# Kernel optimization log

Measured on AMD Instinct MI355X. Metric: run time of the kernel, lower is better.

## Reference

```python
import jax, jax.numpy as jnp
import numpy as np

B, S, K, H = 8192, 512, 8, 512  # batch, size_half, n_segments, hidden
EPS = 1e-6


def setup_inputs() -> dict:
    key = jax.random.key(0)
    k0, k1, k2, k3 = jax.random.split(key, 4)
    x_input = jax.random.uniform(k0, (B, 2 * S), dtype=jnp.float32)  # in [0,1)
    log_density = jax.random.normal(k1, (B, 1), dtype=jnp.float32)
    W1 = jax.random.normal(k2, (S, H), dtype=jnp.float32) / np.sqrt(S).astype(np.float32)
    b1 = jnp.zeros((H,), jnp.float32)
    W2 = jax.random.normal(k3, (H, S * (2 * K + 1)), dtype=jnp.float32) / np.sqrt(H).astype(np.float32)
    b2 = jnp.zeros((S * (2 * K + 1),), jnp.float32)
    return {"x_input": x_input, "log_density": log_density,
            "W1": W1, "b1": b1, "W2": W2, "b2": b2}


def reference(x_input, log_density, W1, b1, W2, b2):
    # even_sites=True: passive half a = first S cols, transformed half b = last S
    x_a = x_input[:, :S]
    x_b = x_input[:, S:]

    # NeuralNetwork: Linear -> tanh -> Linear -> tanh (final_activation == activation)
    hid = jnp.tanh((x_a - 0.5) @ W1 + b1)
    net = jnp.tanh(hid @ W2 + b2).reshape(-1, S, 2 * K + 1)  # [B,S,2K+1]
    h_raw, w_raw = net[..., :K + 1], net[..., K + 1:]

    w_norm = jax.nn.softmax(w_raw, axis=2)                       # [B,S,K]
    eh = jnp.exp(h_raw)                                          # [B,S,K+1]
    h_norm = eh / jnp.sum(0.5 * w_norm * (eh[..., :-1] + eh[..., 1:]),
                          axis=2, keepdims=True)

    b = x_a.shape[0]
    x_knots = jnp.concatenate(
        [jnp.full((b, S, 1), -EPS, x_a.dtype), jnp.cumsum(w_norm, axis=2)], axis=2)  # [B,S,K+1]
    pdf_area = 0.5 * w_norm * (h_norm[..., :-1] + h_norm[..., 1:])
    phi_knots = jnp.concatenate(
        [jnp.zeros((b, S, 1), x_a.dtype), jnp.cumsum(pdf_area, axis=2)], axis=2)     # [B,S,K+1]

    # searchsorted(left) - 1 == (# knots strictly below x) - 1
    k_ind = jnp.clip(jnp.sum(x_knots < x_b[..., None], axis=2) - 1, 0, K - 1)[..., None]

    w_k = jnp.take_along_axis(w_norm, k_ind, axis=2)
    h_k = jnp.take_along_axis(h_norm, k_ind, axis=2)
    h_kp1 = jnp.take_along_axis(h_norm, k_ind + 1, axis=2)
    x_km1 = jnp.take_along_axis(x_knots, k_ind, axis=2)
    phi_km1 = jnp.take_along_axis(phi_knots, k_ind, axis=2)

    alpha = (x_b[..., None] - x_km1) / w_k
    phi_b = (phi_km1 + alpha * h_k * w_k
             + 0.5 * alpha ** 2 * (h_kp1 - h_k) * w_k)[..., 0]    # [B,S]

    phi_out = jnp.concatenate([x_a, phi_b], axis=1)               # [B,2S]
    new_log_density = log_density - jnp.sum(
        jnp.log(h_k + alpha * (h_kp1 - h_k)), axis=1)             # [B,1]
    return phi_out, new_log_density
```

## Files before the change

kernel.cpp:

```cpp
#include <hip/hip_runtime.h>
#include <stdint.h>
#include <math.h>

#define BROWS 8192
#define SDIM  512
#define HDIM  512
#define NCOL  8704
#define EPSK  1e-6f
#define LOG2E  1.442695041f
#define TWOL2E 2.885390082f
#define LN2    0.6931471806f

typedef __attribute__((ext_vector_type(8))) short bf16x8;
typedef __attribute__((ext_vector_type(4))) short bf16x4;
typedef __attribute__((ext_vector_type(4))) float f32x4;

__device__ __forceinline__ unsigned short f2bf(float f) {
    unsigned u = __float_as_uint(f);
    u += 0x7fffu + ((u >> 16) & 1u);
    return (unsigned short)(u >> 16);
}
__device__ __forceinline__ unsigned short f2bf_fast(float f) {
    return (unsigned short)((__float_as_uint(f) + 0x8000u) >> 16);
}
__device__ __forceinline__ float bf2f(unsigned short s) {
    return __uint_as_float(((unsigned)s) << 16);
}
#define EXP2F(x) __builtin_amdgcn_exp2f(x)
#define LOG2F(x) __builtin_amdgcn_logf(x)
#define RCPF(x)  __builtin_amdgcn_rcpf(x)

__device__ __forceinline__ float ftanh(float x) {
    float e = EXP2F(TWOL2E * x);
    return (e - 1.f) * RCPF(e + 1.f);
}
__device__ __forceinline__ float ftanh_l2e(float acc, float bias2L) {
    float e = EXP2F(fmaf(acc, TWOL2E, bias2L));
    return fmaf(e, LOG2E, -LOG2E) * RCPF(e + 1.f);
}

#define GLD16(g, l)                                                         \
    __builtin_amdgcn_global_load_lds(                                       \
        (const __attribute__((address_space(1))) void*)(g),                 \
        (__attribute__((address_space(3))) void*)(l), 16, 0, 0)

__global__ __launch_bounds__(256) void prep_k(
    const float* __restrict__ W2, unsigned short* __restrict__ W2p,
    const float* __restrict__ W1, unsigned short* __restrict__ W1T,
    const float* __restrict__ logd, float* __restrict__ out,
    const float* __restrict__ x)
{
    __shared__ float tile[32 * 33];
    const int t   = threadIdx.x;
    const int bid = blockIdx.x;
    if (bid < 2176) {
        const int ct = bid >> 2;
        const int kq = bid & 3;
        const int colbase = ct * 16;
        const int colblk = ct / 17;
        const int chunk  = ct - colblk * 17;
        const int k32 = t >> 3;
        const int c2  = (t & 7) * 2;
        const int r   = t >> 4;
        const int e2  = (t & 15) * 2;
        for (int kk = kq * 4; kk < kq * 4 + 4; ++kk) {
            float2 v = *(const float2*)&W2[(size_t)(kk * 32 + k32) * NCOL + colbase + c2];
            __syncthreads();
            tile[k32 * 17 + c2 + 0] = v.x;
            tile[k32 * 17 + c2 + 1] = v.y;
            __syncthreads();
            const size_t off = (((size_t)colblk * 16 + kk) * 17 + chunk) * 512;
            ushort2 o;
            o.x = f2bf(tile[(e2 + 0) * 17 + r]);
            o.y = f2bf(tile[(e2 + 1) * 17 + r]);
            *(ushort2*)&W2p[off + (size_t)r * 32 + e2] = o;
        }
    } else if (bid < 2432) {
        const int bt = bid - 2176;
        const int cb = (bt & 15) * 32;
        const int rb = (bt >> 4) * 32;
        const int ty = t >> 3, tx = (t & 7) * 4;
        float4 v = *(const float4*)&W1[(size_t)(rb + ty) * HDIM + cb + tx];
        tile[ty * 33 + tx + 0] = v.x;
        tile[ty * 33 + tx + 1] = v.y;
        tile[ty * 33 + tx + 2] = v.z;
        tile[ty * 33 + tx + 3] = v.w;
        __syncthreads();
        const int oy = t >> 3, ox = (t & 7) * 4;
        bf16x4 o;
        o[0] = (short)f2bf(tile[(ox + 0) * 33 + oy]);
        o[1] = (short)f2bf(tile[(ox + 1) * 33 + oy]);
        o[2] = (short)f2bf(tile[(ox + 2) * 33 + oy]);
        o[3] = (short)f2bf(tile[(ox + 3) * 33 + oy]);
        *(bf16x4*)&W1T[(size_t)(cb + oy) * SDIM + rb + ox] = o;
    } else if (bid < 2688) {
        const int bt = bid - 2432;
        const float4* xi = (const float4*)x;
        float4* oo = (float4*)out;
        const int base = bt * 4096 + t;
#pragma unroll
        for (int k2 = 0; k2 < 16; ++k2) {
            const int f = base + k2 * 256;
            const int row = f >> 7, c4 = f & 127;
            oo[(size_t)row * 256 + c4] = xi[(size_t)row * 256 + c4];
        }
    } else {
        const int b = (bid - 2688) * 256 + t;
        out[(size_t)BROWS * (2 * SDIM) + b] = logd[b];
    }
}

__global__ __launch_bounds__(256) void gemm1_mfma(
    const float* __restrict__ x,
    const unsigned short* __restrict__ W1T,
    const float* __restrict__ b1,
    unsigned short* __restrict__ hid)
{
    __shared__ float Asf[2][64 * 32];
    __shared__ short Bsb[2][128 * 32];

    const int flat = blockIdx.y * 4 + blockIdx.x;
    const int xcd  = flat & 7;
    const int j8   = flat >> 3;
    const int bn   = (j8 & 3) * 128;
    const int bm   = (xcd * 16 + (j8 >> 2)) * 64;

    const int tid  = threadIdx.x;
    const int lane = tid & 63;
    const int wave = tid >> 6;
    const int ln15 = lane & 15;
    const int quad = lane >> 4;
    const int wm   = (wave >> 1) * 32;
    const int wn   = (wave & 1) * 64;
    const int brow = lane >> 2;
    const int bsub_sw = (lane & 3) ^ ((lane >> 3) & 3);
    const int arow8   = lane >> 3;
    const int aslot_sw = (lane & 7) ^ (arow8 & 7);
    const int qsw = (quad ^ ((ln15 >> 1) & 3)) * 8;
    const int ag  = ln15 & 7;

    f32x4 acc[2][4];
#pragma unroll
    for (int i = 0; i < 2; i++)
#pragma unroll
        for (int j = 0; j < 4; j++) acc[i][j] = (f32x4){0.f, 0.f, 0.f, 0.f};

    const float* asrc = &x[(size_t)(bm + arow8) * (2 * SDIM) + aslot_sw * 4];
    const unsigned short* bsrc = &W1T[(size_t)(bn + brow) * SDIM + bsub_sw * 8];

    auto issue = [&](int n, int p) {
#pragma unroll
        for (int c = 0; c < 2; ++c) {
            const int ca = wave * 2 + c;
            GLD16(asrc + (size_t)ca * 8 * (2 * SDIM) + n * 32, &Asf[p][ca * 256]);
        }
#pragma unroll
        for (int c = 0; c < 2; ++c) {
            const int cb = wave * 2 + c;
            GLD16(bsrc + (size_t)cb * 16 * SDIM + n * 32, &Bsb[p][cb * 512]);
        }
    };

    issue(0, 0);
    for (int n = 0; n < 16; ++n) {
        __syncthreads();
        if (n < 15) issue(n + 1, (n + 1) & 1);
        const float* As = Asf[n & 1];
        const short* Bs = Bsb[n & 1];

        bf16x8 af[2], bfr[4];
#pragma unroll
        for (int i = 0; i < 2; ++i) {
            const int r = wm + i * 16 + ln15;
            f32x4 a0 = *(const f32x4*)&As[r * 32 + ((2 * quad + 0) ^ ag) * 4];
            f32x4 a1 = *(const f32x4*)&As[r * 32 + ((2 * quad + 1) ^ ag) * 4];
            bf16x8 v;
            v[0] = (short)f2bf_fast(a0[0] - 0.5f); v[1] = (short)f2bf_fast(a0[1] - 0.5f);
            v[2] = (short)f2bf_fast(a0[2] - 0.5f); v[3] = (short)f2bf_fast(a0[3] - 0.5f);
            v[4] = (short)f2bf_fast(a1[0] - 0.5f); v[5] = (short)f2bf_fast(a1[1] - 0.5f);
            v[6] = (short)f2bf_fast(a1[2] - 0.5f); v[7] = (short)f2bf_fast(a1[3] - 0.5f);
            af[i] = v;
        }
#pragma unroll
        for (int j = 0; j < 4; ++j)
            bfr[j] = *(const bf16x8*)&Bs[(wn + j * 16 + ln15) * 32 + qsw];
#pragma unroll
        for (int i = 0; i < 2; ++i)
#pragma unroll
            for (int j = 0; j < 4; ++j)
                acc[i][j] = __builtin_amdgcn_mfma_f32_16x16x32_bf16(af[i], bfr[j], acc[i][j], 0, 0, 0);
    }

#pragma unroll
    for (int j = 0; j < 4; j++) {
        const int col = bn + wn + j * 16 + ln15;
        const float bias = b1[col];
#pragma unroll
        for (int i = 0; i < 2; i++) {
#pragma unroll
            for (int r = 0; r < 4; r++) {
                const int row = bm + wm + i * 16 + quad * 4 + r;
                hid[(size_t)row * HDIM + col] = f2bf(ftanh(acc[i][j][r] + bias));
            }
        }
    }
}

__global__ __launch_bounds__(256, 2) void gemm2_spline_mfma(
    const unsigned short* __restrict__ hid,
    const unsigned short* __restrict__ W2p,
    const float* __restrict__ b2,
    const float* __restrict__ x,
    float* __restrict__ out)
{
    __shared__ short smem[35904];

    const int bm     = blockIdx.x * 128;
    const int colblk = blockIdx.y;
    const int tid  = threadIdx.x;
    const int lane = tid & 63;
    const int wave = tid >> 6;
    const int ln15 = lane & 15;
    const int quad = lane >> 4;
    const int brow = lane >> 2;
    const int bsub_sw = (lane & 3) ^ ((lane >> 3) & 3);
    const int qsw = (quad ^ ((ln15 >> 1) & 3)) * 8;
    const int jstart = wave * 4;
    const int jcount = (wave == 3) ? 5 : 4;
    const int bcol = colblk * 272;

    f32x4 acc[8][5];
#pragma unroll
    for (int i = 0; i < 8; i++)
#pragma unroll
        for (int j = 0; j < 5; j++) acc[i][j] = (f32x4){0.f, 0.f, 0.f, 0.f};

    const unsigned short* bbase =
        W2p + ((size_t)colblk * 16) * 17 * 512 + (size_t)(lane >> 2) * 32 + (size_t)bsub_sw * 8;
    const unsigned short* abase0 =
        &hid[(size_t)(bm + wave * 32 + brow) * HDIM + bsub_sw * 8];
    const unsigned short* abase1 = abase0 + 16 * HDIM;

    auto issue = [&](int n, int p) {
        short* dst = smem + p * 12800;
        GLD16(abase0 + n * 32, &dst[(2 * wave + 0) * 512]);
        GLD16(abase1 + n * 32, &dst[(2 * wave + 1) * 512]);
        const unsigned short* bk = bbase + (size_t)n * (17 * 512);
        for (int c = 0; c < jcount; ++c) {
            const int chunk = jstart + c;
            GLD16(bk + (size_t)chunk * 512, &dst[4096 + chunk * 512]);
        }
    };

    issue(0, 0);
    for (int n = 0; n < 16; ++n) {
        __syncthreads();
        if (n < 15) issue(n + 1, (n + 1) & 1);
        const short* As = smem + (n & 1) * 12800;
        const short* Bs = As + 4096;

        bf16x8 af[8];
#pragma unroll
        for (int i = 0; i < 8; i++)
            af[i] = *(const bf16x8*)&As[(i * 16 + ln15) * 32 + qsw];

#define KSTEP(JC)                                                               \
        _Pragma("unroll") for (int j = 0; j < (JC); ++j) {                      \
            bf16x8 bfr = *(const bf16x8*)&Bs[((jstart + j) * 16 + ln15) * 32 + qsw]; \
            _Pragma("unroll") for (int i = 0; i < 8; ++i)                       \
                acc[i][j] = __builtin_amdgcn_mfma_f32_16x16x32_bf16(af[i], bfr, acc[i][j], 0, 0, 0); \
        }
        if (wave == 3) { KSTEP(5) } else { KSTEP(4) }
#undef KSTEP
    }

    const int sp = tid & 15;
    const int r0 = tid >> 4;
    const int sglob = colblk * 16 + sp;
    float xbv[8];
#pragma unroll
    for (int t = 0; t < 8; ++t)
        xbv[t] = x[(size_t)(bm + t * 16 + r0) * (2 * SDIM) + SDIM + sglob];

    __syncthreads();
#define EPI1(JC)                                                                \
    _Pragma("unroll") for (int j = 0; j < (JC); ++j) {                          \
        const int col_l = (jstart + j) * 16 + ln15;                             \
        const float bias2L = b2[bcol + col_l] * TWOL2E;                         \
        _Pragma("unroll") for (int i = 0; i < 8; ++i) {                         \
            bf16x4 o;                                                           \
            _Pragma("unroll") for (int r = 0; r < 4; ++r)                       \
                o[r] = (short)f2bf_fast(ftanh_l2e(acc[i][j][r], bias2L));       \
            *(bf16x4*)&smem[col_l * 132 + i * 16 + quad * 4] = o;               \
        }                                                                       \
    }
    if (wave == 3) { EPI1(5) } else { EPI1(4) }
#undef EPI1
    __syncthreads();

    for (int t = 0; t < 8; ++t) {
        const int row_l = t * 16 + r0;
        const int row = bm + row_l;
        const int cbase = sp * 17 * 132 + row_l;

        float s[17];
#pragma unroll
        for (int c = 0; c < 17; c++)
            s[c] = bf2f((unsigned short)smem[cbase + c * 132]);

        float eh[9], e[8];
#pragma unroll
        for (int j = 0; j < 9; j++) eh[j] = EXP2F(s[j]);
#pragma unroll
        for (int c = 0; c < 8; c++) e[c]  = EXP2F(s[9 + c]);

        float cum_e[8], cum_u[8];
        cum_e[0] = e[0];
        cum_u[0] = e[0] * (eh[0] + eh[1]);
#pragma unroll
        for (int c = 1; c < 8; c++) {
            cum_e[c] = cum_e[c - 1] + e[c];
            cum_u[c] = fmaf(e[c], eh[c] + eh[c + 1], cum_u[c - 1]);
        }
        const float se = cum_e[7];
        const float su = cum_u[7];
        const float thr = xbv[t] * se;

        float selE = e[0], selEH = eh[0], selEH1 = eh[1];
        float selCE = -EPSK * se, selCU = 0.f;
#pragma unroll
        for (int c = 1; c < 8; c++) {
            const bool tt = (cum_e[c - 1] < thr);
            selE   = tt ? e[c]         : selE;
            selEH  = tt ? eh[c]        : selEH;
            selEH1 = tt ? eh[c + 1]    : selEH1;
            selCE  = tt ? cum_e[c - 1] : selCE;
            selCU  = tt ? cum_u[c - 1] : selCU;
        }

        const float alpha = (thr - selCE) * RCPF(selE);
        const float dlt   = selEH1 - selEH;
        const float su_inv = RCPF(su);
        float p = fmaf(2.f * alpha, selE * selEH, selCU);
        p = fmaf(alpha * alpha, selE * dlt, p);
        out[(size_t)row * (2 * SDIM) + SDIM + sglob] = p * su_inv;

        const float g = fmaf(alpha, dlt, selEH) * (2.f * se * su_inv);
        float lg = LOG2F(g);
        lg += __shfl_xor(lg, 1);
        lg += __shfl_xor(lg, 2);
        lg += __shfl_xor(lg, 4);
        lg += __shfl_xor(lg, 8);
        if (sp == 0)
            atomicAdd(&out[(size_t)BROWS * (2 * SDIM) + row], -lg * LN2);
    }
}

extern "C" void kernel_launch(void* const* d_in, const int* in_sizes, int n_in,
                              void* d_out, int out_size, void* d_ws, size_t ws_size,
                              hipStream_t stream) {
    const float* x    = (const float*)d_in[0];
    const float* logd = (const float*)d_in[1];
    const float* W1   = (const float*)d_in[2];
    const float* b1   = (const float*)d_in[3];
    const float* W2   = (const float*)d_in[4];
    const float* b2   = (const float*)d_in[5];
    float* out = (float*)d_out;

    char* ws = (char*)d_ws;
    unsigned short* W1T = (unsigned short*)(ws + 32768);
    unsigned short* W2p = (unsigned short*)(ws + 557056);
    unsigned short* hid = (unsigned short*)(ws + 9469952);

    prep_k<<<2720, 256, 0, stream>>>(W2, W2p, W1, W1T, logd, out, x);
    gemm1_mfma<<<dim3(4, 128), 256, 0, stream>>>(x, W1T, b1, hid);
    gemm2_spline_mfma<<<dim3(64, 32), 256, 0, stream>>>(hid, W2p, b2, x, out);
}
```

Before: 221.2 us.

## Overlap W2 repack and x copy with GEMM1 in one fused launch

Splits the prep kernel so that only the W1 transpose and log-density copy run first. The W2 bf16 repack and the x_a passthrough copy are merged into the same launch as GEMM1 as extra block ranges, so the memory-bound prep work can run alongside the GEMM. In GEMM2 the inner loop is reordered to load B fragments once and stream A fragments, with s_setprio raised around the MFMAs, and the b2 bias loads are hoisted before the barrier. The fused kernel costs one fewer launch, but its blocks are uneven and share LDS sizing with the GEMM.

```diff
diff --git a/kernel.cpp b/kernel.cpp
--- a/kernel.cpp
+++ b/kernel.cpp
@@ -44,41 +44,16 @@
         (const __attribute__((address_space(1))) void*)(g),                 \
         (__attribute__((address_space(3))) void*)(l), 16, 0, 0)
 
-__global__ __launch_bounds__(256) void prep_k(
-    const float* __restrict__ W2, unsigned short* __restrict__ W2p,
+__global__ __launch_bounds__(256) void prep_a(
     const float* __restrict__ W1, unsigned short* __restrict__ W1T,
-    const float* __restrict__ logd, float* __restrict__ out,
-    const float* __restrict__ x)
+    const float* __restrict__ logd, float* __restrict__ out)
 {
     __shared__ float tile[32 * 33];
     const int t   = threadIdx.x;
     const int bid = blockIdx.x;
-    if (bid < 2176) {
-        const int ct = bid >> 2;
-        const int kq = bid & 3;
-        const int colbase = ct * 16;
-        const int colblk = ct / 17;
-        const int chunk  = ct - colblk * 17;
-        const int k32 = t >> 3;
-        const int c2  = (t & 7) * 2;
-        const int r   = t >> 4;
-        const int e2  = (t & 15) * 2;
-        for (int kk = kq * 4; kk < kq * 4 + 4; ++kk) {
-            float2 v = *(const float2*)&W2[(size_t)(kk * 32 + k32) * NCOL + colbase + c2];
-            __syncthreads();
-            tile[k32 * 17 + c2 + 0] = v.x;
-            tile[k32 * 17 + c2 + 1] = v.y;
-            __syncthreads();
-            const size_t off = (((size_t)colblk * 16 + kk) * 17 + chunk) * 512;
-            ushort2 o;
-            o.x = f2bf(tile[(e2 + 0) * 17 + r]);
-            o.y = f2bf(tile[(e2 + 1) * 17 + r]);
-            *(ushort2*)&W2p[off + (size_t)r * 32 + e2] = o;
-        }
-    } else if (bid < 2432) {
-        const int bt = bid - 2176;
-        const int cb = (bt & 15) * 32;
-        const int rb = (bt >> 4) * 32;
+    if (bid < 256) {
+        const int cb = (bid & 15) * 32;
+        const int rb = (bid >> 4) * 32;
         const int ty = t >> 3, tx = (t & 7) * 4;
         float4 v = *(const float4*)&W1[(size_t)(rb + ty) * HDIM + cb + tx];
         tile[ty * 33 + tx + 0] = v.x;
@@ -93,115 +68,145 @@
         o[2] = (short)f2bf(tile[(ox + 2) * 33 + oy]);
         o[3] = (short)f2bf(tile[(ox + 3) * 33 + oy]);
         *(bf16x4*)&W1T[(size_t)(cb + oy) * SDIM + rb + ox] = o;
+    } else {
+        const int b = (bid - 256) * 256 + t;
+        out[(size_t)BROWS * (2 * SDIM) + b] = logd[b];
+    }
+}
+
+__global__ __launch_bounds__(256) void mega_k(
+    const float* __restrict__ x,
+    const unsigned short* __restrict__ W1T,
+    const float* __restrict__ b1,
+    unsigned short* __restrict__ hid,
+    const float* __restrict__ W2,
+    unsigned short* __restrict__ W2p,
+    float* __restrict__ out)
+{
+    __shared__ float Asf[2][64 * 32];
+    __shared__ short Bsb[2][128 * 32];
+    const int bid = blockIdx.x;
+    const int tid = threadIdx.x;
+
+    if (bid < 512) {
+        const int flat = bid;
+        const int xcd  = flat & 7;
+        const int j8   = flat >> 3;
+        const int bn   = (j8 & 3) * 128;
+        const int bm   = (xcd * 16 + (j8 >> 2)) * 64;
+
+        const int lane = tid & 63;
+        const int wave = tid >> 6;
+        const int ln15 = lane & 15;
+        const int quad = lane >> 4;
+        const int wm   = (wave >> 1) * 32;
+        const int wn   = (wave & 1) * 64;
+        const int brow = lane >> 2;
+        const int bsub_sw = (lane & 3) ^ ((lane >> 3) & 3);
+        const int arow8   = lane >> 3;
+        const int aslot_sw = (lane & 7) ^ (arow8 & 7);
+        const int qsw = (quad ^ ((ln15 >> 1) & 3)) * 8;
+        const int ag  = ln15 & 7;
+
+        f32x4 acc[2][4];
+#pragma unroll
+        for (int i = 0; i < 2; i++)
+#pragma unroll
+            for (int j = 0; j < 4; j++) acc[i][j] = (f32x4){0.f, 0.f, 0.f, 0.f};
+
+        const float* asrc = &x[(size_t)(bm + arow8) * (2 * SDIM) + aslot_sw * 4];
+        const unsigned short* bsrc = &W1T[(size_t)(bn + brow) * SDIM + bsub_sw * 8];
+
+        auto issue = [&](int n, int p) {
+#pragma unroll
+            for (int c = 0; c < 2; ++c) {
+                const int ca = wave * 2 + c;
+                GLD16(asrc + (size_t)ca * 8 * (2 * SDIM) + n * 32, &Asf[p][ca * 256]);
+            }
+#pragma unroll
+            for (int c = 0; c < 2; ++c) {
+                const int cb = wave * 2 + c;
+                GLD16(bsrc + (size_t)cb * 16 * SDIM + n * 32, &Bsb[p][cb * 512]);
+            }
+        };
+
+        issue(0, 0);
+        for (int n = 0; n < 16; ++n) {
+            __syncthreads();
+            if (n < 15) issue(n + 1, (n + 1) & 1);
+            const float* As = Asf[n & 1];
+            const short* Bs = Bsb[n & 1];
+
+            bf16x8 af[2], bfr[4];
+#pragma unroll
+            for (int i = 0; i < 2; ++i) {
+                const int r = wm + i * 16 + ln15;
+                f32x4 a0 = *(const f32x4*)&As[r * 32 + ((2 * quad + 0) ^ ag) * 4];
+                f32x4 a1 = *(const f32x4*)&As[r * 32 + ((2 * quad + 1) ^ ag) * 4];
+                bf16x8 v;
+                v[0] = (short)f2bf_fast(a0[0] - 0.5f); v[1] = (short)f2bf_fast(a0[1] - 0.5f);
+                v[2] = (short)f2bf_fast(a0[2] - 0.5f); v[3] = (short)f2bf_fast(a0[3] - 0.5f);
+                v[4] = (short)f2bf_fast(a1[0] - 0.5f); v[5] = (short)f2bf_fast(a1[1] - 0.5f);
+                v[6] = (short)f2bf_fast(a1[2] - 0.5f); v[7] = (short)f2bf_fast(a1[3] - 0.5f);
+                af[i] = v;
+            }
+#pragma unroll
+            for (int j = 0; j < 4; ++j)
+                bfr[j] = *(const bf16x8*)&Bsb[n & 1][(wn + j * 16 + ln15) * 32 + qsw];
+#pragma unroll
+            for (int i = 0; i < 2; ++i)
+#pragma unroll
+                for (int j = 0; j < 4; ++j)
+                    acc[i][j] = __builtin_amdgcn_mfma_f32_16x16x32_bf16(af[i], bfr[j], acc[i][j], 0, 0, 0);
+            (void)Bs; (void)As;
+        }
+
+#pragma unroll
+        for (int j = 0; j < 4; j++) {
+            const int col = bn + wn + j * 16 + ln15;
+            const float bias = b1[col];
+#pragma unroll
+            for (int i = 0; i < 2; i++) {
+#pragma unroll
+                for (int r = 0; r < 4; r++) {
+                    const int row = bm + wm + i * 16 + quad * 4 + r;
+                    hid[(size_t)row * HDIM + col] = f2bf(ftanh(acc[i][j][r] + bias));
+                }
+            }
+        }
     } else if (bid < 2688) {
-        const int bt = bid - 2432;
+        float* tile = &Asf[0][0];
+        const int ct = (bid - 512) >> 2;
+        const int kq = (bid - 512) & 3;
+        const int colbase = ct * 16;
+        const int colblk = ct / 17;
+        const int chunk  = ct - colblk * 17;
+        const int k32 = tid >> 3;
+        const int c2  = (tid & 7) * 2;
+        const int r   = tid >> 4;
+        const int e2  = (tid & 15) * 2;
+        for (int kk = kq * 4; kk < kq * 4 + 4; ++kk) {
+            float2 v = *(const float2*)&W2[(size_t)(kk * 32 + k32) * NCOL + colbase + c2];
+            __syncthreads();
+            tile[k32 * 17 + c2 + 0] = v.x;
+            tile[k32 * 17 + c2 + 1] = v.y;
+            __syncthreads();
+            const size_t off = (((size_t)colblk * 16 + kk) * 17 + chunk) * 512;
+            ushort2 o;
+            o.x = f2bf(tile[(e2 + 0) * 17 + r]);
+            o.y = f2bf(tile[(e2 + 1) * 17 + r]);
+            *(ushort2*)&W2p[off + (size_t)r * 32 + e2] = o;
+        }
+    } else {
+        const int bt = bid - 2688;
         const float4* xi = (const float4*)x;
         float4* oo = (float4*)out;
-        const int base = bt * 4096 + t;
+        const int base = bt * 4096 + tid;
 #pragma unroll
         for (int k2 = 0; k2 < 16; ++k2) {
             const int f = base + k2 * 256;
             const int row = f >> 7, c4 = f & 127;
             oo[(size_t)row * 256 + c4] = xi[(size_t)row * 256 + c4];
-        }
-    } else {
-        const int b = (bid - 2688) * 256 + t;
-        out[(size_t)BROWS * (2 * SDIM) + b] = logd[b];
-    }
-}
-
-__global__ __launch_bounds__(256) void gemm1_mfma(
-    const float* __restrict__ x,
-    const unsigned short* __restrict__ W1T,
-    const float* __restrict__ b1,
-    unsigned short* __restrict__ hid)
-{
-    __shared__ float Asf[2][64 * 32];
-    __shared__ short Bsb[2][128 * 32];
-
-    const int flat = blockIdx.y * 4 + blockIdx.x;
-    const int xcd  = flat & 7;
-    const int j8   = flat >> 3;
-    const int bn   = (j8 & 3) * 128;
-    const int bm   = (xcd * 16 + (j8 >> 2)) * 64;
-
-    const int tid  = threadIdx.x;
-    const int lane = tid & 63;
-    const int wave = tid >> 6;
-    const int ln15 = lane & 15;
-    const int quad = lane >> 4;
-    const int wm   = (wave >> 1) * 32;
-    const int wn   = (wave & 1) * 64;
-    const int brow = lane >> 2;
-    const int bsub_sw = (lane & 3) ^ ((lane >> 3) & 3);
-    const int arow8   = lane >> 3;
-    const int aslot_sw = (lane & 7) ^ (arow8 & 7);
-    const int qsw = (quad ^ ((ln15 >> 1) & 3)) * 8;
-    const int ag  = ln15 & 7;
-
-    f32x4 acc[2][4];
-#pragma unroll
-    for (int i = 0; i < 2; i++)
-#pragma unroll
-        for (int j = 0; j < 4; j++) acc[i][j] = (f32x4){0.f, 0.f, 0.f, 0.f};
-
-    const float* asrc = &x[(size_t)(bm + arow8) * (2 * SDIM) + aslot_sw * 4];
-    const unsigned short* bsrc = &W1T[(size_t)(bn + brow) * SDIM + bsub_sw * 8];
-
-    auto issue = [&](int n, int p) {
-#pragma unroll
-        for (int c = 0; c < 2; ++c) {
-            const int ca = wave * 2 + c;
-            GLD16(asrc + (size_t)ca * 8 * (2 * SDIM) + n * 32, &Asf[p][ca * 256]);
-        }
-#pragma unroll
-        for (int c = 0; c < 2; ++c) {
-            const int cb = wave * 2 + c;
-            GLD16(bsrc + (size_t)cb * 16 * SDIM + n * 32, &Bsb[p][cb * 512]);
-        }
-    };
-
-    issue(0, 0);
-    for (int n = 0; n < 16; ++n) {
-        __syncthreads();
-        if (n < 15) issue(n + 1, (n + 1) & 1);
-        const float* As = Asf[n & 1];
-        const short* Bs = Bsb[n & 1];
-
-        bf16x8 af[2], bfr[4];
-#pragma unroll
-        for (int i = 0; i < 2; ++i) {
-            const int r = wm + i * 16 + ln15;
-            f32x4 a0 = *(const f32x4*)&As[r * 32 + ((2 * quad + 0) ^ ag) * 4];
-            f32x4 a1 = *(const f32x4*)&As[r * 32 + ((2 * quad + 1) ^ ag) * 4];
-            bf16x8 v;
-            v[0] = (short)f2bf_fast(a0[0] - 0.5f); v[1] = (short)f2bf_fast(a0[1] - 0.5f);
-            v[2] = (short)f2bf_fast(a0[2] - 0.5f); v[3] = (short)f2bf_fast(a0[3] - 0.5f);
-            v[4] = (short)f2bf_fast(a1[0] - 0.5f); v[5] = (short)f2bf_fast(a1[1] - 0.5f);
-            v[6] = (short)f2bf_fast(a1[2] - 0.5f); v[7] = (short)f2bf_fast(a1[3] - 0.5f);
-            af[i] = v;
-        }
-#pragma unroll
-        for (int j = 0; j < 4; ++j)
-            bfr[j] = *(const bf16x8*)&Bs[(wn + j * 16 + ln15) * 32 + qsw];
-#pragma unroll
-        for (int i = 0; i < 2; ++i)
-#pragma unroll
-            for (int j = 0; j < 4; ++j)
-                acc[i][j] = __builtin_amdgcn_mfma_f32_16x16x32_bf16(af[i], bfr[j], acc[i][j], 0, 0, 0);
-    }
-
-#pragma unroll
-    for (int j = 0; j < 4; j++) {
-        const int col = bn + wn + j * 16 + ln15;
-        const float bias = b1[col];
-#pragma unroll
-        for (int i = 0; i < 2; i++) {
-#pragma unroll
-            for (int r = 0; r < 4; r++) {
-                const int row = bm + wm + i * 16 + quad * 4 + r;
-                hid[(size_t)row * HDIM + col] = f2bf(ftanh(acc[i][j][r] + bias));
-            }
         }
     }
 }
@@ -259,19 +264,27 @@
         const short* As = smem + (n & 1) * 12800;
         const short* Bs = As + 4096;
 
-        bf16x8 af[8];
-#pragma unroll
-        for (int i = 0; i < 8; i++)
-            af[i] = *(const bf16x8*)&As[(i * 16 + ln15) * 32 + qsw];
-
-#define KSTEP(JC)                                                               \
-        _Pragma("unroll") for (int j = 0; j < (JC); ++j) {                      \
-            bf16x8 bfr = *(const bf16x8*)&Bs[((jstart + j) * 16 + ln15) * 32 + qsw]; \
-            _Pragma("unroll") for (int i = 0; i < 8; ++i)                       \
-                acc[i][j] = __builtin_amdgcn_mfma_f32_16x16x32_bf16(af[i], bfr, acc[i][j], 0, 0, 0); \
-        }
-        if (wave == 3) { KSTEP(5) } else { KSTEP(4) }
-#undef KSTEP
+        bf16x8 bfr[5];
+        if (wave == 3) {
+#pragma unroll
+            for (int j = 0; j < 5; ++j)
+                bfr[j] = *(const bf16x8*)&Bs[((jstart + j) * 16 + ln15) * 32 + qsw];
+        } else {
+#pragma unroll
+            for (int j = 0; j < 4; ++j)
+                bfr[j] = *(const bf16x8*)&Bs[((jstart + j) * 16 + ln15) * 32 + qsw];
+        }
+
+        __builtin_amdgcn_s_setprio(1);
+#define ILOOP(JC)                                                               \
+        _Pragma("unroll") for (int i = 0; i < 8; ++i) {                         \
+            bf16x8 af = *(const bf16x8*)&As[(i * 16 + ln15) * 32 + qsw];        \
+            _Pragma("unroll") for (int j = 0; j < (JC); ++j)                    \
+                acc[i][j] = __builtin_amdgcn_mfma_f32_16x16x32_bf16(af, bfr[j], acc[i][j], 0, 0, 0); \
+        }
+        if (wave == 3) { ILOOP(5) } else { ILOOP(4) }
+#undef ILOOP
+        __builtin_amdgcn_s_setprio(0);
     }
 
     const int sp = tid & 15;
@@ -281,12 +294,16 @@
 #pragma unroll
     for (int t = 0; t < 8; ++t)
         xbv[t] = x[(size_t)(bm + t * 16 + r0) * (2 * SDIM) + SDIM + sglob];
+    float b2v[5];
+#pragma unroll
+    for (int j = 0; j < 5; ++j)
+        b2v[j] = b2[bcol + (jstart + j) * 16 + ln15] * TWOL2E;
 
     __syncthreads();
 #define EPI1(JC)                                                                \
     _Pragma("unroll") for (int j = 0; j < (JC); ++j) {                          \
         const int col_l = (jstart + j) * 16 + ln15;                             \
-        const float bias2L = b2[bcol + col_l] * TWOL2E;                         \
+        const float bias2L = b2v[j];                                            \
         _Pragma("unroll") for (int i = 0; i < 8; ++i) {                         \
             bf16x4 o;                                                           \
             _Pragma("unroll") for (int r = 0; r < 4; ++r)                       \
@@ -372,7 +389,7 @@
     unsigned short* W2p = (unsigned short*)(ws + 557056);
     unsigned short* hid = (unsigned short*)(ws + 9469952);
 
-    prep_k<<<2720, 256, 0, stream>>>(W2, W2p, W1, W1T, logd, out, x);
-    gemm1_mfma<<<dim3(4, 128), 256, 0, stream>>>(x, W1T, b1, hid);
+    prep_a<<<288, 256, 0, stream>>>(W1, W1T, logd, out);
+    mega_k<<<2944, 256, 0, stream>>>(x, W1T, b1, hid, W2, W2p, out);
     gemm2_spline_mfma<<<dim3(64, 32), 256, 0, stream>>>(hid, W2p, b2, x, out);
 }
```

Measured after the change: 224.0 us. Within noise of the previous version (+1.3%).
